# Kernel optimization log

Measured on AMD Instinct MI355X. Metric: run time of the kernel, lower is better.

Reference implementation:

```python
import jax, jax.numpy as jnp
import numpy as np

HEIGHT = 8  # output crop height (module init arg)


def setup_inputs() -> dict:
    key = jax.random.key(0)
    k = jax.random.split(key, 8)
    N, Himg, Wimg, C = 16, 512, 512, 3
    M = 8192  # total boxes across the batch
    images = jax.random.normal(k[0], (N, Himg, Wimg, C), jnp.float32)
    feature_map = jax.random.normal(k[1], (N, 128, 128, 32), jnp.float32)
    # boxes: (x1, y1, x2, y2, angle); sized so width = HEIGHT*bw/bh <= 60 < max_width=64
    x1 = jax.random.uniform(k[2], (M,), minval=0.0, maxval=392.0)
    y1 = jax.random.uniform(k[3], (M,), minval=0.0, maxval=448.0)
    bw = jax.random.uniform(k[4], (M,), minval=16.0, maxval=120.0)
    bh = jax.random.uniform(k[5], (M,), minval=16.0, maxval=64.0)
    ang = jax.random.uniform(k[6], (M,), minval=-0.785, maxval=0.785)
    boxes = jnp.stack([x1, y1, x1 + bw, y1 + bh, ang], axis=-1)
    box_indices = jax.random.randint(k[7], (M,), 0, N).astype(jnp.int32)
    return {"images": images, "feature_map": feature_map, "boxes": boxes,
            "box_indices": box_indices, "max_width": 64}


def _roi_rotate(images, boxes, box_indices, max_width):
    """Rotated crop-and-resize with bilinear sampling.
    Returns crops [M, HEIGHT, max_width, C] (zero-padded past each box's width)
    and the per-box float output widths [M]."""
    Himg, Wimg = images.shape[1], images.shape[2]
    x1, y1, x2, y2, ang = (boxes[:, i] for i in range(5))
    bw, bh = x2 - x1, y2 - y1
    width = HEIGHT * bw / bh                      # per-box output width (float)
    cx, cy = (x1 + x2) * 0.5, (y1 + y2) * 0.5     # box center
    s = (bh / HEIGHT)[:, None, None]              # uniform scale (src px per dst px)

    ii = jnp.arange(HEIGHT, dtype=images.dtype)[None, :, None]      # [1,H,1]
    jj = jnp.arange(max_width, dtype=images.dtype)[None, None, :]   # [1,1,W]
    w_ = width[:, None, None]
    dx = s * (jj - (w_ - 1.0) * 0.5)              # [M,H,W] local offsets
    dy = s * (ii - (HEIGHT - 1.0) * 0.5)
    ca = jnp.cos(ang)[:, None, None]
    sa = jnp.sin(ang)[:, None, None]
    sx = cx[:, None, None] + ca * dx - sa * dy    # rotated source coords
    sy = cy[:, None, None] + sa * dx + ca * dy

    x0 = jnp.floor(sx)
    y0 = jnp.floor(sy)
    fx = (sx - x0)[..., None]
    fy = (sy - y0)[..., None]
    x0i = jnp.clip(x0, 0, Wimg - 1).astype(jnp.int32)
    x1i = jnp.clip(x0 + 1.0, 0, Wimg - 1).astype(jnp.int32)
    y0i = jnp.clip(y0, 0, Himg - 1).astype(jnp.int32)
    y1i = jnp.clip(y0 + 1.0, 0, Himg - 1).astype(jnp.int32)

    b = box_indices[:, None, None]                # [M,1,1] broadcasts to [M,H,W]
    v00 = images[b, y0i, x0i]                     # [M,H,W,C] irregular gathers
    v01 = images[b, y0i, x1i]
    v10 = images[b, y1i, x0i]
    v11 = images[b, y1i, x1i]
    out = (v00 * (1 - fx) * (1 - fy) + v01 * fx * (1 - fy)
           + v10 * (1 - fx) * fy + v11 * fx * fy)

    # zero outside the image and past each box's actual width (padding)
    valid = ((jj < jnp.ceil(w_)) & (sx >= 0) & (sx <= Wimg - 1)
             & (sy >= 0) & (sy <= Himg - 1))
    crops = out * valid[..., None].astype(out.dtype)
    return crops, width


def reference(images, feature_map, boxes, box_indices, max_width):
    # feature_map is accepted (forward signature) but, per the source, crops
    # are taken from `images`.
    crops, width = _roi_rotate(images, boxes, box_indices, max_width)
    boxes_padded_width = max_width - width
    return crops, boxes_padded_width
```

## Files before the change

### kernel.cpp

```cpp
#include <hip/hip_runtime.h>

#define HEIGHT 8

__global__ void __launch_bounds__(512)
roi_rotate_kernel(const float* __restrict__ images,
                  const float* __restrict__ boxes,
                  const int* __restrict__ box_indices,
                  float* __restrict__ crops,
                  float* __restrict__ width_out,
                  int max_width, int Himg, int Wimg)
{
    const int m   = blockIdx.x;
    const int tid = threadIdx.x;
    const int i   = tid / max_width;
    const int j   = tid - i * max_width;

    __shared__ float p[6];
    if (tid == 0) {
        float x1  = boxes[m * 5 + 0];
        float y1  = boxes[m * 5 + 1];
        float x2  = boxes[m * 5 + 2];
        float y2  = boxes[m * 5 + 3];
        float ang = boxes[m * 5 + 4];
        float bw = x2 - x1, bh = y2 - y1;
        float width = (float)HEIGHT * bw / bh;
        p[0] = (x1 + x2) * 0.5f;
        p[1] = (y1 + y2) * 0.5f;
        p[2] = bh / (float)HEIGHT;
        p[3] = width;
        p[4] = cosf(ang);
        p[5] = sinf(ang);
        width_out[m] = (float)max_width - width;
    }
    __syncthreads();
    const float cx = p[0], cy = p[1], s = p[2], width = p[3], ca = p[4], sa = p[5];

    const float dx = s * ((float)j - (width  - 1.0f) * 0.5f);
    const float dy = s * ((float)i - ((float)HEIGHT - 1.0f) * 0.5f);
    const float sx = cx + ca * dx - sa * dy;
    const float sy = cy + sa * dx + ca * dy;

    float* o = crops + ((size_t)(m * HEIGHT + i) * max_width + j) * 3;

    const bool valid = ((float)j < ceilf(width)) &&
                       (sx >= 0.0f) && (sx <= (float)(Wimg - 1)) &&
                       (sy >= 0.0f) && (sy <= (float)(Himg - 1));

    if (!valid) {
        o[0] = 0.0f; o[1] = 0.0f; o[2] = 0.0f;
        return;
    }

    const float x0 = floorf(sx);
    const float y0 = floorf(sy);
    const float fx = sx - x0;
    const float fy = sy - y0;
    const int x0i = (int)fminf(fmaxf(x0,        0.0f), (float)(Wimg - 1));
    const int x1i = (int)fminf(fmaxf(x0 + 1.0f, 0.0f), (float)(Wimg - 1));
    const int y0i = (int)fminf(fmaxf(y0,        0.0f), (float)(Himg - 1));
    const int y1i = (int)fminf(fmaxf(y0 + 1.0f, 0.0f), (float)(Himg - 1));

    const int b = box_indices[m];
    const float* img = images + (size_t)b * Himg * Wimg * 3;
    const size_t o00 = ((size_t)y0i * Wimg + x0i) * 3;
    const size_t o01 = ((size_t)y0i * Wimg + x1i) * 3;
    const size_t o10 = ((size_t)y1i * Wimg + x0i) * 3;
    const size_t o11 = ((size_t)y1i * Wimg + x1i) * 3;

    const float w00 = (1.0f - fx) * (1.0f - fy);
    const float w01 = fx * (1.0f - fy);
    const float w10 = (1.0f - fx) * fy;
    const float w11 = fx * fy;

    #pragma unroll
    for (int c = 0; c < 3; ++c) {
        float v = images ? 0.0f : 0.0f;
        v = img[o00 + c] * w00 + img[o01 + c] * w01 +
            img[o10 + c] * w10 + img[o11 + c] * w11;
        o[c] = v;
    }
}

extern "C" void kernel_launch(void* const* d_in, const int* in_sizes, int n_in,
                              void* d_out, int out_size, void* d_ws, size_t ws_size,
                              hipStream_t stream) {
    const float* images      = (const float*)d_in[0];
    const float* boxes       = (const float*)d_in[2];
    const int*   box_indices = (const int*)d_in[3];

    const int M  = in_sizes[3];
    const int mw = (out_size - M) / (M * HEIGHT * 3);
    const int Himg = 512, Wimg = 512;

    float* crops     = (float*)d_out;
    float* width_out = crops + (size_t)M * HEIGHT * mw * 3;

    dim3 block(HEIGHT * mw);
    dim3 grid(M);
    roi_rotate_kernel<<<grid, block, 0, stream>>>(images, boxes, box_indices,
                                                  crops, width_out, mw, Himg, Wimg);
}
```

Baseline: 37.56 us.

## Stage crop outputs in LDS for float4 stores and remap threads column-major

Every thread now computes the box parameters itself, which removes the thread-0 shared-memory broadcast and its barrier. Threads are remapped so that consecutive lanes walk down the 8 rows of one column, which tends to put their bilinear gathers closer together in the image. Results are staged through a padded LDS tile so each block can write its contiguous output with coalesced float4 stores instead of strided 3-float writes. This adds a barrier and LDS traffic. The LDS buffer is sized for max_width up to 64, and the (1.0f - fx) arithmetic is duplicated across threads.

```diff
diff --git a/kernel.cpp b/kernel.cpp
--- a/kernel.cpp
+++ b/kernel.cpp
@@ -12,72 +12,86 @@
 {
     const int m   = blockIdx.x;
     const int tid = threadIdx.x;
-    const int i   = tid / max_width;
-    const int j   = tid - i * max_width;
+    const int mw  = max_width;
 
-    __shared__ float p[6];
-    if (tid == 0) {
-        float x1  = boxes[m * 5 + 0];
-        float y1  = boxes[m * 5 + 1];
-        float x2  = boxes[m * 5 + 2];
-        float y2  = boxes[m * 5 + 3];
-        float ang = boxes[m * 5 + 4];
-        float bw = x2 - x1, bh = y2 - y1;
-        float width = (float)HEIGHT * bw / bh;
-        p[0] = (x1 + x2) * 0.5f;
-        p[1] = (y1 + y2) * 0.5f;
-        p[2] = bh / (float)HEIGHT;
-        p[3] = width;
-        p[4] = cosf(ang);
-        p[5] = sinf(ang);
-        width_out[m] = (float)max_width - width;
-    }
-    __syncthreads();
-    const float cx = p[0], cy = p[1], s = p[2], width = p[3], ca = p[4], sa = p[5];
+    const float x1  = boxes[m * 5 + 0];
+    const float y1  = boxes[m * 5 + 1];
+    const float x2  = boxes[m * 5 + 2];
+    const float y2  = boxes[m * 5 + 3];
+    const float ang = boxes[m * 5 + 4];
+    const float bwd = x2 - x1, bhd = y2 - y1;
+    const float width = (float)HEIGHT * bwd / bhd;
+    const float cx = (x1 + x2) * 0.5f;
+    const float cy = (y1 + y2) * 0.5f;
+    const float s  = bhd / (float)HEIGHT;
+    const float ca = cosf(ang);
+    const float sa = sinf(ang);
 
-    const float dx = s * ((float)j - (width  - 1.0f) * 0.5f);
+    if (tid == 0) width_out[m] = (float)mw - width;
+
+    const int i = tid & (HEIGHT - 1);
+    const int j = tid >> 3;
+
+    const float dx = s * ((float)j - (width - 1.0f) * 0.5f);
     const float dy = s * ((float)i - ((float)HEIGHT - 1.0f) * 0.5f);
     const float sx = cx + ca * dx - sa * dy;
     const float sy = cy + sa * dx + ca * dy;
 
-    float* o = crops + ((size_t)(m * HEIGHT + i) * max_width + j) * 3;
+    float v0 = 0.0f, v1 = 0.0f, v2 = 0.0f;
 
     const bool valid = ((float)j < ceilf(width)) &&
                        (sx >= 0.0f) && (sx <= (float)(Wimg - 1)) &&
                        (sy >= 0.0f) && (sy <= (float)(Himg - 1));
 
-    if (!valid) {
-        o[0] = 0.0f; o[1] = 0.0f; o[2] = 0.0f;
-        return;
+    if (valid) {
+        const float x0 = floorf(sx);
+        const float y0 = floorf(sy);
+        const float fx = sx - x0;
+        const float fy = sy - y0;
+        const int x0i = (int)fminf(fmaxf(x0,        0.0f), (float)(Wimg - 1));
+        const int x1i = (int)fminf(fmaxf(x0 + 1.0f, 0.0f), (float)(Wimg - 1));
+        const int y0i = (int)fminf(fmaxf(y0,        0.0f), (float)(Himg - 1));
+        const int y1i = (int)fminf(fmaxf(y0 + 1.0f, 0.0f), (float)(Himg - 1));
+
+        const int b = box_indices[m];
+        const float* img = images + (size_t)b * Himg * Wimg * 3;
+        const size_t o00 = ((size_t)y0i * Wimg + x0i) * 3;
+        const size_t o01 = ((size_t)y0i * Wimg + x1i) * 3;
+        const size_t o10 = ((size_t)y1i * Wimg + x0i) * 3;
+        const size_t o11 = ((size_t)y1i * Wimg + x1i) * 3;
+
+        const float w00 = (1.0f - fx) * (1.0f - fy);
+        const float w01 = fx * (1.0f - fy);
+        const float w10 = (1.0f - fx) * fy;
+        const float w11 = fx * fy;
+
+        v0 = img[o00 + 0] * w00 + img[o01 + 0] * w01 +
+             img[o10 + 0] * w10 + img[o11 + 0] * w11;
+        v1 = img[o00 + 1] * w00 + img[o01 + 1] * w01 +
+             img[o10 + 1] * w10 + img[o11 + 1] * w11;
+        v2 = img[o00 + 2] * w00 + img[o01 + 2] * w01 +
+             img[o10 + 2] * w10 + img[o11 + 2] * w11;
     }
 
-    const float x0 = floorf(sx);
-    const float y0 = floorf(sy);
-    const float fx = sx - x0;
-    const float fy = sy - y0;
-    const int x0i = (int)fminf(fmaxf(x0,        0.0f), (float)(Wimg - 1));
-    const int x1i = (int)fminf(fmaxf(x0 + 1.0f, 0.0f), (float)(Wimg - 1));
-    const int y0i = (int)fminf(fmaxf(y0,        0.0f), (float)(Himg - 1));
-    const int y1i = (int)fminf(fmaxf(y0 + 1.0f, 0.0f), (float)(Himg - 1));
+    __shared__ float lds[HEIGHT * (64 * 3 + 4)];
+    const int STRIDE = 3 * mw + 4;
+    float* dst = &lds[i * STRIDE + j * 3];
+    dst[0] = v0; dst[1] = v1; dst[2] = v2;
+    __syncthreads();
 
-    const int b = box_indices[m];
-    const float* img = images + (size_t)b * Himg * Wimg * 3;
-    const size_t o00 = ((size_t)y0i * Wimg + x0i) * 3;
-    const size_t o01 = ((size_t)y0i * Wimg + x1i) * 3;
-    const size_t o10 = ((size_t)y1i * Wimg + x0i) * 3;
-    const size_t o11 = ((size_t)y1i * Wimg + x1i) * 3;
-
-    const float w00 = (1.0f - fx) * (1.0f - fy);
-    const float w01 = fx * (1.0f - fy);
-    const float w10 = (1.0f - fx) * fy;
-    const float w11 = fx * fy;
-
-    #pragma unroll
-    for (int c = 0; c < 3; ++c) {
-        float v = images ? 0.0f : 0.0f;
-        v = img[o00 + c] * w00 + img[o01 + c] * w01 +
-            img[o10 + c] * w10 + img[o11 + c] * w11;
-        o[c] = v;
+    float* oblk = crops + (size_t)m * HEIGHT * mw * 3;
+    if ((mw & 3) == 0) {
+        const int nf4 = (HEIGHT * mw * 3) >> 2;
+        if (tid < nf4) {
+            const int f   = tid * 4;
+            const int ii  = f / (3 * mw);
+            const int rem = f - ii * (3 * mw);
+            const float4 val = *(const float4*)&lds[ii * STRIDE + rem];
+            *(float4*)&oblk[f] = val;
+        }
+    } else {
+        float* o = oblk + ((size_t)i * mw + j) * 3;
+        o[0] = v0; o[1] = v1; o[2] = v2;
     }
 }
 
```

Result: no change. 37.79 us (+0.6%).
